# Kernel optimization log

Hardware: AMD Instinct MI355X
Metric: run time of the kernel (lower is better)

The kernel has to match this reference:

```python
import jax, jax.numpy as jnp
import numpy as np

LLR_CLIP = 20.0   # allowed_llr_range(abs=20)
QMAX = 7.5        # decoder_qms_qbit = 5 -> round(x*2)/2, clip +/-7.5


def _quantize_ste(x):
    # straight-through quantizer: forward = quantized, grad flows through clipped x
    q = jnp.clip(jnp.round(x * 2.0) / 2.0, -QMAX, QMAX)
    xc = jnp.clip(x, -QMAX, QMAX)
    return xc + jax.lax.stop_gradient(q - xc)


def _decode(xa, cn_weights, vn_idx, cn_idx, shifts, M):
    # xa: (B, Z, N) channel LLRs; messages live on lifted edges (B, Z, E)
    B, Z, N = xa.shape
    E = vn_idx.shape[0]
    iters = cn_weights.shape[0]

    zidx = jnp.arange(Z)
    lift = (zidx[:, None] + shifts[None, :]) % Z    # VN-domain -> CN-domain cyclic shift per edge
    unlift = (zidx[:, None] - shifts[None, :]) % Z  # inverse shift
    lift_b = jnp.broadcast_to(lift[None], (B, Z, E))
    unlift_b = jnp.broadcast_to(unlift[None], (B, Z, E))

    V = jax.nn.one_hot(vn_idx, N, dtype=xa.dtype)   # (E, N) edge->VN incidence (= W_output / W_skipconn2even)
    eids = jnp.arange(E)
    llr_e = xa[:, :, vn_idx]                        # per-edge channel LLR (B, Z, E)

    c2v = jnp.zeros((B, Z, E), xa.dtype)
    for it in range(iters):
        # --- VN update (odd layer): extrinsic sum + channel LLR, clipped ---
        tot = jnp.einsum('bze,en->bzn', c2v, V)                 # per-VN sum of incoming c2v
        v2c = jnp.clip(llr_e + tot[:, :, vn_idx] - c2v, -LLR_CLIP, LLR_CLIP)

        # --- lift to CN domain (Lift_Matrix1) ---
        m = jnp.take_along_axis(v2c, lift_b, axis=1)            # (B, Z, E)
        mt = m.transpose(2, 0, 1).reshape(E, B * Z)             # edges leading for segment ops

        # --- CN update (even layer): extrinsic min-sum via two-min trick ---
        a = jnp.abs(mt)
        neg = (mt < 0).astype(jnp.int32)
        min1 = jax.ops.segment_min(a, cn_idx, num_segments=M)               # (M, B*Z)
        ismin = a == min1[cn_idx]
        first = jax.ops.segment_min(jnp.where(ismin, eids[:, None], E),
                                    cn_idx, num_segments=M)                 # tie-break by edge id
        isfirst = eids[:, None] == first[cn_idx]
        min2 = jax.ops.segment_min(jnp.where(isfirst, jnp.inf, a),
                                   cn_idx, num_segments=M)
        ext_min = jnp.where(isfirst, min2[cn_idx], min1[cn_idx])
        negtot = jax.ops.segment_sum(neg, cn_idx, num_segments=M)
        sgn = (1 - 2 * ((negtot[cn_idx] - neg) % 2)).astype(mt.dtype)       # extrinsic sign product

        msg = _quantize_ste(cn_weights[it] * sgn * ext_min)     # per-iteration scalar CN weight + QMS quantize

        # --- unlift back to VN domain (Lift_Matrix2) ---
        mc = msg.reshape(E, B, Z).transpose(1, 2, 0)
        c2v = jnp.take_along_axis(mc, unlift_b, axis=1)

    # marginal output LLRs (W_output): channel + all incoming c2v, shape (B, N*Z)
    out = xa + jnp.einsum('bze,en->bzn', c2v, V)
    return out.transpose(0, 2, 1).reshape(B, N * Z)


def setup_inputs() -> dict:
    key = jax.random.key(0)
    B, Z, N, M, dc = 32, 384, 68, 46, 7
    E = M * dc  # 322
    k1, k2, k3 = jax.random.split(key, 3)
    xa = jax.random.normal(k1, (B, Z, N), dtype=jnp.float32) * 4.0
    cn_weights = jnp.ones((8,), jnp.float32)
    cn_idx = jnp.repeat(jnp.arange(M), dc)                      # regular CN degree 7
    vn_idx = jax.random.randint(k2, (E,), 0, N)
    shifts = jax.random.randint(k3, (E,), 0, Z)
    return {"xa": xa, "cn_weights": cn_weights, "vn_idx": vn_idx,
            "cn_idx": cn_idx, "shifts": shifts, "M": M}


def reference(xa, cn_weights, vn_idx, cn_idx, shifts, M):
    return _decode(xa, cn_weights, vn_idx, cn_idx, shifts, M)
```

## Files before the change

kernel.cpp:

```cpp
#include <hip/hip_runtime.h>

#define B_   32
#define Z_   384
#define N_   68
#define M_   46
#define DC_  7
#define E_   (M_ * DC_)
#define ZN   (Z_ * N_)
#define ZM   (Z_ * M_)

#define XAT_OFF   0
#define LT_OFF    (B_ * ZN)
#define MSG_OFF   (2 * B_ * ZN)
#define EVS_OFF   (MSG_OFF + 2 * B_ * ZM)
#define OFFS_OFF  (EVS_OFF + E_)
#define LST_OFF   (OFFS_OFF + N_ + 1)
#define WS_INTS   (LST_OFF + E_)


__global__ __launch_bounds__(384)
void k_pre_tables(const float* __restrict__ xa,
                  const int* __restrict__ vn_idx, const int* __restrict__ shifts,
                  int* __restrict__ ws, float* __restrict__ xat_dst)
{
    const int tid = threadIdx.x;
    if (blockIdx.x == B_ * 6) {
        __shared__ int evs[E_];
        __shared__ int offs[N_ + 1];
        __shared__ int lists[E_];
        if (tid < E_) evs[tid] = vn_idx[tid] | (shifts[tid] << 7);
        __syncthreads();
        if (tid < N_) {
            int c = 0;
            for (int e = 0; e < E_; ++e) c += ((evs[e] & 127) == tid);
            offs[tid + 1] = c;
        }
        if (tid == 0) offs[0] = 0;
        __syncthreads();
        if (tid == 0) { for (int n = 0; n < N_; ++n) offs[n + 1] += offs[n]; }
        __syncthreads();
        if (tid < N_) {
            int p = offs[tid];
            for (int e = 0; e < E_; ++e) {
                int rec = evs[e];
                if ((rec & 127) == tid) {
                    int s = rec >> 7;
                    lists[p++] = s | ((e / DC_) << 9) | ((e % DC_) << 15);
                }
            }
        }
        __syncthreads();
        if (tid < E_) { ws[EVS_OFF + tid] = evs[tid]; ws[LST_OFF + tid] = lists[tid]; }
        if (tid < N_ + 1) ws[OFFS_OFF + tid] = offs[tid];
        return;
    }
    __shared__ float tile[N_ * 65];
    const int x = blockIdx.x & 7;
    const int k = blockIdx.x >> 3;
    const int b = x + 8 * (k & 3);
    const int t = k >> 2;
    const int z0 = t * 64;
    const float* src = xa + (size_t)b * ZN + (size_t)z0 * N_;
    for (int i = tid; i < 64 * N_; i += 384) {
        int r = i / N_, n = i - r * N_;
        tile[n * 65 + r] = src[i];
    }
    __syncthreads();
    float* dst = xat_dst + (size_t)b * ZN + z0;
    for (int i = tid; i < 64 * N_; i += 384) {
        int n = i >> 6, zl = i & 63;
        dst[n * Z_ + zl] = tile[n * 65 + zl];
    }
}

__global__ __launch_bounds__(384)
void k_passB(const float* __restrict__ cw, const int* __restrict__ ws_tbl,
             int2* __restrict__ msg, const float* __restrict__ src_g,
             int it, int use_init)
{
    __shared__ int cevs[DC_];
    const int x = blockIdx.x & 7;
    const int k = blockIdx.x >> 3;
    const int b = x + 8 * (k & 3);
    const int m = k >> 2;
    const int z = threadIdx.x;
    if (z < DC_) cevs[z] = ws_tbl[EVS_OFF + m * DC_ + z];
    __syncthreads();

    const float* src = src_g + (size_t)b * ZN;
    int2* mp = msg + (size_t)b * ZM + m * Z_;
    const int2 old = use_init ? make_int2(0, 0) : mp[z];
    const float w = cw[it];

    float m1 = 1e30f, m2 = 1e30f;
    int f = 0, negb = 0;
    #pragma unroll
    for (int j = 0; j < DC_; ++j) {
        int rec = cevs[j];
        int vn = rec & 127;
        int s  = rec >> 7;
        int zr = z + s; if (zr >= Z_) zr -= Z_;
        int w32 = (j < 4) ? old.x : old.y;
        int c2 = (w32 << (24 - 8 * (j & 3))) >> 24;
        float v = src[vn * Z_ + zr] - 0.5f * (float)c2;
        v = fminf(fmaxf(v, -20.0f), 20.0f);
        negb |= (v < 0.0f) << j;
        float a = fabsf(v);
        if (a < m1) { m2 = m1; m1 = a; f = j; }
        else if (a < m2) { m2 = a; }
    }
    float r1 = fminf(fmaxf(rintf(w * m1 * 2.0f), -15.0f), 15.0f);
    float r2 = fminf(fmaxf(rintf(w * m2 * 2.0f), -15.0f), 15.0f);
    const int q1 = (int)r1, q2 = (int)r2;
    const int par = __popc(negb);
    int lo = 0, hi = 0;
    #pragma unroll
    for (int j = 0; j < DC_; ++j) {
        int q  = (j == f) ? q2 : q1;
        int sj = (par - ((negb >> j) & 1)) & 1;
        int mj = sj ? -q : q;
        if (j < 4) lo |= (mj & 255) << (8 * j);
        else       hi |= (mj & 255) << (8 * (j - 4));
    }
    mp[z] = make_int2(lo, hi);
}

__global__ __launch_bounds__(384)
void k_passA(const float* __restrict__ xat, const int* __restrict__ ws_tbl,
             const int2* __restrict__ msg, float* __restrict__ dst)
{
    __shared__ int vlist[E_];
    __shared__ int s_cnt;
    const int x = blockIdx.x & 7;
    const int k = blockIdx.x >> 3;
    const int b = x + 8 * (k & 3);
    const int n = k >> 2;
    const int tid = threadIdx.x;
    if (tid == 0) s_cnt = ws_tbl[OFFS_OFF + n + 1] - ws_tbl[OFFS_OFF + n];
    {
        int o = ws_tbl[OFFS_OFF + n];
        int e = ws_tbl[OFFS_OFF + n + 1];
        for (int q = o + tid; q < e; q += 384) vlist[q - o] = ws_tbl[LST_OFF + q];
    }
    __syncthreads();

    const int z = tid;
    const signed char* mb = (const signed char*)(msg + (size_t)b * ZM);
    const int cnt = s_cnt;
    int t2 = 0;
    for (int q = 0; q < cnt; ++q) {
        int rec = vlist[q];
        int s = rec & 511;
        int m = (rec >> 9) & 63;
        int j = (rec >> 15) & 7;
        int zs = z - s; if (zs < 0) zs += Z_;
        t2 += (int)mb[((m * Z_ + zs) << 3) + j];
    }
    dst[(size_t)b * ZN + n * Z_ + z] =
        xat[(size_t)b * ZN + n * Z_ + z] + 0.5f * (float)t2;
}

#define INIT_STATE ((16u << 10) | (16u << 15))
__device__ __forceinline__ int decode2(unsigned st, int j) {
    int neg   = (st >> j) & 1;
    int q1    = (int)((st >> 10) & 31) - 16;
    int q2    = (int)((st >> 15) & 31) - 16;
    int first = (int)((st >> 7) & 7);
    int q     = (j == first) ? q2 : q1;
    int par   = (__popc(st & 127u) - neg) & 1;
    return par ? -q : q;
}

__global__ __launch_bounds__(1024)
void ldpc_decode_kernel(const float* __restrict__ xa,
                        const float* __restrict__ cw,
                        const int*   __restrict__ vn_idx,
                        const int*   __restrict__ shifts,
                        float* out, int iters)
{
    __shared__ short tot[ZN];
    __shared__ int   evs[E_];
    __shared__ int   offs[N_ + 1];
    __shared__ int   lists[E_];
    __shared__ float wlds[8];

    const int tid = threadIdx.x;
    const int b   = blockIdx.x;
    const float* xab = xa + (size_t)b * ZN;
    float* outb = out + (size_t)b * ZN;
    int* stateg = (int*)outb;

    if (tid < E_) evs[tid] = vn_idx[tid] | (shifts[tid] << 7);
    if (tid < iters && tid < 8) wlds[tid] = cw[tid];
    __syncthreads();
    if (tid < N_) {
        int c = 0;
        for (int e = 0; e < E_; ++e) c += ((evs[e] & 127) == tid);
        offs[tid + 1] = c;
    }
    if (tid == 0) offs[0] = 0;
    __syncthreads();
    if (tid == 0) { for (int n = 0; n < N_; ++n) offs[n + 1] += offs[n]; }
    __syncthreads();
    if (tid < N_) {
        int p = offs[tid];
        for (int e = 0; e < E_; ++e) {
            int rec = evs[e];
            if ((rec & 127) == tid) {
                int s = rec >> 7;
                lists[p++] = s | ((e / DC_) << 9) | ((e % DC_) << 15);
            }
        }
    }
    __syncthreads();

    for (int i = tid; i < ZM; i += 1024) stateg[i] = (int)INIT_STATE;
    __syncthreads();

    for (int it = 0; it < iters; ++it) {
        for (int i = tid; i < ZN; i += 1024) {
            int z = i / N_, n = i - z * N_, t2 = 0;
            int kend = offs[n + 1];
            for (int k = offs[n]; k < kend; ++k) {
                int rec = lists[k];
                int s = rec & 511, m = (rec >> 9) & 63, j = rec >> 15;
                int zs = z - s; if (zs < 0) zs += Z_;
                t2 += decode2((unsigned)stateg[zs * M_ + m], j);
            }
            tot[i] = (short)t2;
        }
        __syncthreads();
        const float w = wlds[it];
        for (int i = tid; i < ZM; i += 1024) {
            int z = i / M_, m = i - z * M_;
            unsigned st = (unsigned)stateg[i];
            float m1 = 1e30f, m2 = 1e30f;
            int f = 0, negb = 0;
            #pragma unroll
            for (int j = 0; j < DC_; ++j) {
                int rec = evs[m * DC_ + j];
                int vn = rec & 127, s = rec >> 7;
                int zr = z + s; if (zr >= Z_) zr -= Z_;
                int c2 = decode2(st, j);
                int idx = zr * N_ + vn;
                float v = (xab[idx] + 0.5f * (float)tot[idx]) - 0.5f * (float)c2;
                v = fminf(fmaxf(v, -20.0f), 20.0f);
                negb |= (v < 0.0f) << j;
                float a = fabsf(v);
                if (a < m1) { m2 = m1; m1 = a; f = j; }
                else if (a < m2) { m2 = a; }
            }
            float r1 = fminf(fmaxf(rintf(w * m1 * 2.0f), -15.0f), 15.0f);
            float r2 = fminf(fmaxf(rintf(w * m2 * 2.0f), -15.0f), 15.0f);
            stateg[i] = (int)(unsigned)(negb | (f << 7) | (((int)r1 + 16) << 10) | (((int)r2 + 16) << 15));
        }
        __syncthreads();
    }

    for (int i = tid; i < ZN; i += 1024) {
        int z = i / N_, n = i - z * N_, t2 = 0;
        int kend = offs[n + 1];
        for (int k = offs[n]; k < kend; ++k) {
            int rec = lists[k];
            int s = rec & 511, m = (rec >> 9) & 63, j = rec >> 15;
            int zs = z - s; if (zs < 0) zs += Z_;
            t2 += decode2((unsigned)stateg[zs * M_ + m], j);
        }
        tot[i] = (short)t2;
    }
    __syncthreads();
    for (int i = tid; i < ZN; i += 1024) {
        int n = i / Z_, z = i - n * Z_;
        outb[i] = xab[z * N_ + n] + 0.5f * (float)tot[z * N_ + n];
    }
}

extern "C" void kernel_launch(void* const* d_in, const int* in_sizes, int n_in,
                              void* d_out, int out_size, void* d_ws, size_t ws_size,
                              hipStream_t stream) {
    const float* xa = (const float*)d_in[0];
    const float* cw = (const float*)d_in[1];
    const int* vn   = (const int*)d_in[2];
    const int* sh   = (const int*)d_in[4];
    int iters = in_sizes[1];
    float* outp = (float*)d_out;

    if (ws_size >= (size_t)WS_INTS * sizeof(int)) {
        int*   ws  = (int*)d_ws;
        float* xat = (float*)d_ws + XAT_OFF;
        float* lt  = (float*)d_ws + LT_OFF;
        int2*  msg = (int2*)(ws + MSG_OFF);

        if (iters == 0) {
            hipLaunchKernelGGL(k_pre_tables, dim3(B_ * 6 + 1), dim3(384), 0, stream,
                               xa, vn, sh, ws, outp);
            return;
        }
        hipLaunchKernelGGL(k_pre_tables, dim3(B_ * 6 + 1), dim3(384), 0, stream,
                           xa, vn, sh, ws, xat);
        hipLaunchKernelGGL(k_passB, dim3(B_ * M_), dim3(384), 0, stream,
                           cw, ws, msg, xat, 0, 1);
        for (int it = 1; it < iters; ++it) {
            hipLaunchKernelGGL(k_passA, dim3(B_ * N_), dim3(384), 0, stream,
                               xat, ws, msg, lt);
            hipLaunchKernelGGL(k_passB, dim3(B_ * M_), dim3(384), 0, stream,
                               cw, ws, msg, lt, it, 0);
        }
        hipLaunchKernelGGL(k_passA, dim3(B_ * N_), dim3(384), 0, stream,
                           xat, ws, msg, outp);
    } else {
        hipLaunchKernelGGL(ldpc_decode_kernel, dim3(B_), dim3(1024), 0, stream,
                           xa, cw, vn, sh, outp, iters);
    }
}
```

Baseline: 202.0 us.

## Replace per-iteration kernel launches with a persistent cooperative kernel using grid barriers

The per-iteration passA/passB launch sequence is replaced by one cooperative persistent kernel of 256 blocks × 1024 threads. Each block handles one slice of one batch and alternates VN and CN passes, separated by an atomic-counter grid barrier stored in the workspace. The aim is to remove the launch overhead and inter-kernel gaps of about 16 small launches. In exchange, each pass now runs on fewer blocks with a strided loop, and every phase pays barrier spin latency. Correctness depends on all 256 blocks being co-resident.

```diff
diff --git a/kernel.cpp b/kernel.cpp
--- a/kernel.cpp
+++ b/kernel.cpp
@@ -8,6 +8,9 @@
 #define E_   (M_ * DC_)
 #define ZN   (Z_ * N_)
 #define ZM   (Z_ * M_)
+#define GB_  256
+#define ZN_S (ZN / 8)
+#define ZM_S (ZM / 8)
 
 #define XAT_OFF   0
 #define LT_OFF    (B_ * ZN)
@@ -15,7 +18,8 @@
 #define EVS_OFF   (MSG_OFF + 2 * B_ * ZM)
 #define OFFS_OFF  (EVS_OFF + E_)
 #define LST_OFF   (OFFS_OFF + N_ + 1)
-#define WS_INTS   (LST_OFF + E_)
+#define BAR_OFF   (LST_OFF + E_)
+#define WS_INTS   (BAR_OFF + 2)
 
 
 __global__ __launch_bounds__(384)
@@ -29,6 +33,7 @@
         __shared__ int offs[N_ + 1];
         __shared__ int lists[E_];
         if (tid < E_) evs[tid] = vn_idx[tid] | (shifts[tid] << 7);
+        if (tid == 0) { ws[BAR_OFF] = 0; ws[BAR_OFF + 1] = 0; }
         __syncthreads();
         if (tid < N_) {
             int c = 0;
@@ -73,91 +78,135 @@
     }
 }
 
-__global__ __launch_bounds__(384)
-void k_passB(const float* __restrict__ cw, const int* __restrict__ ws_tbl,
-             int2* __restrict__ msg, const float* __restrict__ src_g,
-             int it, int use_init)
-{
-    __shared__ int cevs[DC_];
-    const int x = blockIdx.x & 7;
-    const int k = blockIdx.x >> 3;
-    const int b = x + 8 * (k & 3);
-    const int m = k >> 2;
-    const int z = threadIdx.x;
-    if (z < DC_) cevs[z] = ws_tbl[EVS_OFF + m * DC_ + z];
-    __syncthreads();
-
+__device__ __forceinline__ void gbar(unsigned* cnt, unsigned* gen, unsigned phase)
+{
+    __syncthreads();
+    if (threadIdx.x == 0) {
+        __threadfence();
+        unsigned old = __hip_atomic_fetch_add(cnt, 1u, __ATOMIC_ACQ_REL,
+                                              __HIP_MEMORY_SCOPE_AGENT);
+        if (old == (unsigned)gridDim.x - 1u) {
+            __hip_atomic_store(cnt, 0u, __ATOMIC_RELAXED, __HIP_MEMORY_SCOPE_AGENT);
+            __hip_atomic_store(gen, phase, __ATOMIC_RELEASE, __HIP_MEMORY_SCOPE_AGENT);
+        } else {
+            while (__hip_atomic_load(gen, __ATOMIC_ACQUIRE,
+                                     __HIP_MEMORY_SCOPE_AGENT) < phase) {
+                __builtin_amdgcn_s_sleep(2);
+            }
+        }
+        __threadfence();
+    }
+    __syncthreads();
+}
+
+__device__ __forceinline__ void passB_slice(int b, int sl,
+                                            const float* __restrict__ src_g,
+                                            int2* __restrict__ msg, float w,
+                                            const int* __restrict__ evs,
+                                            int use_init, int tid)
+{
     const float* src = src_g + (size_t)b * ZN;
-    int2* mp = msg + (size_t)b * ZM + m * Z_;
-    const int2 old = use_init ? make_int2(0, 0) : mp[z];
-    const float w = cw[it];
-
-    float m1 = 1e30f, m2 = 1e30f;
-    int f = 0, negb = 0;
-    #pragma unroll
-    for (int j = 0; j < DC_; ++j) {
-        int rec = cevs[j];
-        int vn = rec & 127;
-        int s  = rec >> 7;
-        int zr = z + s; if (zr >= Z_) zr -= Z_;
-        int w32 = (j < 4) ? old.x : old.y;
-        int c2 = (w32 << (24 - 8 * (j & 3))) >> 24;
-        float v = src[vn * Z_ + zr] - 0.5f * (float)c2;
-        v = fminf(fmaxf(v, -20.0f), 20.0f);
-        negb |= (v < 0.0f) << j;
-        float a = fabsf(v);
-        if (a < m1) { m2 = m1; m1 = a; f = j; }
-        else if (a < m2) { m2 = a; }
-    }
-    float r1 = fminf(fmaxf(rintf(w * m1 * 2.0f), -15.0f), 15.0f);
-    float r2 = fminf(fmaxf(rintf(w * m2 * 2.0f), -15.0f), 15.0f);
-    const int q1 = (int)r1, q2 = (int)r2;
-    const int par = __popc(negb);
-    int lo = 0, hi = 0;
-    #pragma unroll
-    for (int j = 0; j < DC_; ++j) {
-        int q  = (j == f) ? q2 : q1;
-        int sj = (par - ((negb >> j) & 1)) & 1;
-        int mj = sj ? -q : q;
-        if (j < 4) lo |= (mj & 255) << (8 * j);
-        else       hi |= (mj & 255) << (8 * (j - 4));
-    }
-    mp[z] = make_int2(lo, hi);
-}
-
-__global__ __launch_bounds__(384)
-void k_passA(const float* __restrict__ xat, const int* __restrict__ ws_tbl,
-             const int2* __restrict__ msg, float* __restrict__ dst)
-{
-    __shared__ int vlist[E_];
-    __shared__ int s_cnt;
-    const int x = blockIdx.x & 7;
-    const int k = blockIdx.x >> 3;
-    const int b = x + 8 * (k & 3);
-    const int n = k >> 2;
+    int2* mpb = msg + (size_t)b * ZM;
+    const int lo = sl * ZM_S, hi = lo + ZM_S;
+    for (int l = lo + tid; l < hi; l += 1024) {
+        const int m = l / Z_;
+        const int z = l - m * Z_;
+        const int2 old = use_init ? make_int2(0, 0) : mpb[l];
+
+        float m1 = 1e30f, m2 = 1e30f;
+        int f = 0, negb = 0;
+        #pragma unroll
+        for (int j = 0; j < DC_; ++j) {
+            int rec = evs[m * DC_ + j];
+            int vn = rec & 127;
+            int s  = rec >> 7;
+            int zr = z + s; if (zr >= Z_) zr -= Z_;
+            int w32 = (j < 4) ? old.x : old.y;
+            int c2 = (w32 << (24 - 8 * (j & 3))) >> 24;
+            float v = src[vn * Z_ + zr] - 0.5f * (float)c2;
+            v = fminf(fmaxf(v, -20.0f), 20.0f);
+            negb |= (v < 0.0f) << j;
+            float a = fabsf(v);
+            if (a < m1) { m2 = m1; m1 = a; f = j; }
+            else if (a < m2) { m2 = a; }
+        }
+        float r1 = fminf(fmaxf(rintf(w * m1 * 2.0f), -15.0f), 15.0f);
+        float r2 = fminf(fmaxf(rintf(w * m2 * 2.0f), -15.0f), 15.0f);
+        const int q1 = (int)r1, q2 = (int)r2;
+        const int par = __popc(negb);
+        int plo = 0, phi = 0;
+        #pragma unroll
+        for (int j = 0; j < DC_; ++j) {
+            int q  = (j == f) ? q2 : q1;
+            int sj = (par - ((negb >> j) & 1)) & 1;
+            int mj = sj ? -q : q;
+            if (j < 4) plo |= (mj & 255) << (8 * j);
+            else       phi |= (mj & 255) << (8 * (j - 4));
+        }
+        mpb[l] = make_int2(plo, phi);
+    }
+}
+
+__device__ __forceinline__ void passA_slice(int b, int sl,
+                                            const float* __restrict__ xat,
+                                            const int2* __restrict__ msg,
+                                            float* __restrict__ dst,
+                                            const int* __restrict__ offs,
+                                            const int* __restrict__ lists, int tid)
+{
+    const signed char* mb = (const signed char*)(msg + (size_t)b * ZM);
+    const float* xb = xat + (size_t)b * ZN;
+    float* db = dst + (size_t)b * ZN;
+    const int lo = sl * ZN_S, hi = lo + ZN_S;
+    for (int l = lo + tid; l < hi; l += 1024) {
+        const int n = l / Z_;
+        const int z = l - n * Z_;
+        const int o = offs[n], e = offs[n + 1];
+        int t2 = 0;
+        for (int k = o; k < e; ++k) {
+            int rec = lists[k];
+            int s = rec & 511;
+            int m = (rec >> 9) & 63;
+            int j = (rec >> 15) & 7;
+            int zs = z - s; if (zs < 0) zs += Z_;
+            t2 += (int)mb[((m * Z_ + zs) << 3) + j];
+        }
+        db[l] = xb[l] + 0.5f * (float)t2;
+    }
+}
+
+__global__ __launch_bounds__(1024)
+void k_persist(const float* __restrict__ xat, const float* __restrict__ cw,
+               int* __restrict__ ws, int2* __restrict__ msg,
+               float* __restrict__ lt, float* __restrict__ out, int iters)
+{
+    __shared__ int evs[E_];
+    __shared__ int lists[E_];
+    __shared__ int offs[N_ + 1];
+    __shared__ float wlds[8];
     const int tid = threadIdx.x;
-    if (tid == 0) s_cnt = ws_tbl[OFFS_OFF + n + 1] - ws_tbl[OFFS_OFF + n];
-    {
-        int o = ws_tbl[OFFS_OFF + n];
-        int e = ws_tbl[OFFS_OFF + n + 1];
-        for (int q = o + tid; q < e; q += 384) vlist[q - o] = ws_tbl[LST_OFF + q];
-    }
-    __syncthreads();
-
-    const int z = tid;
-    const signed char* mb = (const signed char*)(msg + (size_t)b * ZM);
-    const int cnt = s_cnt;
-    int t2 = 0;
-    for (int q = 0; q < cnt; ++q) {
-        int rec = vlist[q];
-        int s = rec & 511;
-        int m = (rec >> 9) & 63;
-        int j = (rec >> 15) & 7;
-        int zs = z - s; if (zs < 0) zs += Z_;
-        t2 += (int)mb[((m * Z_ + zs) << 3) + j];
-    }
-    dst[(size_t)b * ZN + n * Z_ + z] =
-        xat[(size_t)b * ZN + n * Z_ + z] + 0.5f * (float)t2;
+    if (tid < E_) { evs[tid] = ws[EVS_OFF + tid]; lists[tid] = ws[LST_OFF + tid]; }
+    if (tid < N_ + 1) offs[tid] = ws[OFFS_OFF + tid];
+    if (tid < 8 && tid < iters) wlds[tid] = cw[tid];
+    __syncthreads();
+
+    const int x  = blockIdx.x & 7;
+    const int kk = blockIdx.x >> 3;
+    const int b  = x + 8 * (kk & 3);
+    const int sl = kk >> 2;
+    unsigned* cnt = (unsigned*)(ws + BAR_OFF);
+    unsigned* gen = (unsigned*)(ws + BAR_OFF + 1);
+    unsigned phase = 0;
+
+    passB_slice(b, sl, xat, msg, wlds[0], evs, 1, tid);
+    for (int it = 1; it < iters; ++it) {
+        gbar(cnt, gen, ++phase);
+        passA_slice(b, sl, xat, msg, lt, offs, lists, tid);
+        gbar(cnt, gen, ++phase);
+        passB_slice(b, sl, lt, msg, wlds[it], evs, 0, tid);
+    }
+    gbar(cnt, gen, ++phase);
+    passA_slice(b, sl, xat, msg, out, offs, lists, tid);
 }
 
 #define INIT_STATE ((16u << 10) | (16u << 15))
@@ -298,16 +347,10 @@
         }
         hipLaunchKernelGGL(k_pre_tables, dim3(B_ * 6 + 1), dim3(384), 0, stream,
                            xa, vn, sh, ws, xat);
-        hipLaunchKernelGGL(k_passB, dim3(B_ * M_), dim3(384), 0, stream,
-                           cw, ws, msg, xat, 0, 1);
-        for (int it = 1; it < iters; ++it) {
-            hipLaunchKernelGGL(k_passA, dim3(B_ * N_), dim3(384), 0, stream,
-                               xat, ws, msg, lt);
-            hipLaunchKernelGGL(k_passB, dim3(B_ * M_), dim3(384), 0, stream,
-                               cw, ws, msg, lt, it, 0);
-        }
-        hipLaunchKernelGGL(k_passA, dim3(B_ * N_), dim3(384), 0, stream,
-                           xat, ws, msg, outp);
+        void* args[] = { (void*)&xat, (void*)&cw, (void*)&ws, (void*)&msg,
+                         (void*)&lt, (void*)&outp, (void*)&iters };
+        hipLaunchCooperativeKernel((const void*)k_persist, dim3(GB_), dim3(1024),
+                                   args, 0, stream);
     } else {
         hipLaunchKernelGGL(ldpc_decode_kernel, dim3(B_), dim3(1024), 0, stream,
                            xa, cw, vn, sh, outp, iters);
```

Result: slower. 665.6 us (+229.4%).

## Store CN messages as planar int8 arrays per edge slot, precompute offsets

Applied to the files above, without the earlier changes.

Replaces the packed int2 per-(b,m,z) message layout, eight bytes with one padding, by a planar byte layout indexed by edge slot j, then m, then z. The tables now carry precomputed base offsets (vn*Z, j*ZM+m*Z) so both passes skip the unpacking arithmetic. passA's byte gathers become contiguous across z, so reads coalesce instead of using a stride of eight bytes. The cost is that passB now issues seven separate byte loads and stores per thread instead of one 8-byte access.

```diff
diff --git a/kernel.cpp b/kernel.cpp
--- a/kernel.cpp
+++ b/kernel.cpp
@@ -8,11 +8,13 @@
 #define E_   (M_ * DC_)
 #define ZN   (Z_ * N_)
 #define ZM   (Z_ * M_)
+#define MSB  (DC_ * ZM)
 
 #define XAT_OFF   0
 #define LT_OFF    (B_ * ZN)
 #define MSG_OFF   (2 * B_ * ZN)
-#define EVS_OFF   (MSG_OFF + 2 * B_ * ZM)
+#define MSG_INTS  ((B_ * MSB + 3) / 4)
+#define EVS_OFF   (MSG_OFF + MSG_INTS)
 #define OFFS_OFF  (EVS_OFF + E_)
 #define LST_OFF   (OFFS_OFF + N_ + 1)
 #define WS_INTS   (LST_OFF + E_)
@@ -25,33 +27,33 @@
 {
     const int tid = threadIdx.x;
     if (blockIdx.x == B_ * 6) {
-        __shared__ int evs[E_];
+        __shared__ int vnl[E_];
+        __shared__ int shl[E_];
         __shared__ int offs[N_ + 1];
-        __shared__ int lists[E_];
-        if (tid < E_) evs[tid] = vn_idx[tid] | (shifts[tid] << 7);
+        if (tid < E_) { vnl[tid] = vn_idx[tid]; shl[tid] = shifts[tid]; }
         __syncthreads();
         if (tid < N_) {
             int c = 0;
-            for (int e = 0; e < E_; ++e) c += ((evs[e] & 127) == tid);
+            for (int e = 0; e < E_; ++e) c += (vnl[e] == tid);
             offs[tid + 1] = c;
         }
         if (tid == 0) offs[0] = 0;
         __syncthreads();
         if (tid == 0) { for (int n = 0; n < N_; ++n) offs[n + 1] += offs[n]; }
         __syncthreads();
+        if (tid < E_) {
+            ws[EVS_OFF + tid] = (vnl[tid] * Z_ << 9) | shl[tid];
+        }
+        if (tid < N_ + 1) ws[OFFS_OFF + tid] = offs[tid];
         if (tid < N_) {
             int p = offs[tid];
             for (int e = 0; e < E_; ++e) {
-                int rec = evs[e];
-                if ((rec & 127) == tid) {
-                    int s = rec >> 7;
-                    lists[p++] = s | ((e / DC_) << 9) | ((e % DC_) << 15);
+                if (vnl[e] == tid) {
+                    int m = e / DC_, j = e - m * DC_;
+                    ws[LST_OFF + p++] = ((j * ZM + m * Z_) << 9) | shl[e];
                 }
             }
         }
-        __syncthreads();
-        if (tid < E_) { ws[EVS_OFF + tid] = evs[tid]; ws[LST_OFF + tid] = lists[tid]; }
-        if (tid < N_ + 1) ws[OFFS_OFF + tid] = offs[tid];
         return;
     }
     __shared__ float tile[N_ * 65];
@@ -75,7 +77,7 @@
 
 __global__ __launch_bounds__(384)
 void k_passB(const float* __restrict__ cw, const int* __restrict__ ws_tbl,
-             int2* __restrict__ msg, const float* __restrict__ src_g,
+             signed char* __restrict__ msg, const float* __restrict__ src_g,
              int it, int use_init)
 {
     __shared__ int cevs[DC_];
@@ -88,8 +90,7 @@
     __syncthreads();
 
     const float* src = src_g + (size_t)b * ZN;
-    int2* mp = msg + (size_t)b * ZM + m * Z_;
-    const int2 old = use_init ? make_int2(0, 0) : mp[z];
+    signed char* mp = msg + (size_t)b * MSB + m * Z_ + z;
     const float w = cw[it];
 
     float m1 = 1e30f, m2 = 1e30f;
@@ -97,12 +98,10 @@
     #pragma unroll
     for (int j = 0; j < DC_; ++j) {
         int rec = cevs[j];
-        int vn = rec & 127;
-        int s  = rec >> 7;
+        int s = rec & 511;
         int zr = z + s; if (zr >= Z_) zr -= Z_;
-        int w32 = (j < 4) ? old.x : old.y;
-        int c2 = (w32 << (24 - 8 * (j & 3))) >> 24;
-        float v = src[vn * Z_ + zr] - 0.5f * (float)c2;
+        int c2 = use_init ? 0 : (int)mp[j * ZM];
+        float v = src[(rec >> 9) + zr] - 0.5f * (float)c2;
         v = fminf(fmaxf(v, -20.0f), 20.0f);
         negb |= (v < 0.0f) << j;
         float a = fabsf(v);
@@ -113,48 +112,40 @@
     float r2 = fminf(fmaxf(rintf(w * m2 * 2.0f), -15.0f), 15.0f);
     const int q1 = (int)r1, q2 = (int)r2;
     const int par = __popc(negb);
-    int lo = 0, hi = 0;
     #pragma unroll
     for (int j = 0; j < DC_; ++j) {
         int q  = (j == f) ? q2 : q1;
         int sj = (par - ((negb >> j) & 1)) & 1;
-        int mj = sj ? -q : q;
-        if (j < 4) lo |= (mj & 255) << (8 * j);
-        else       hi |= (mj & 255) << (8 * (j - 4));
-    }
-    mp[z] = make_int2(lo, hi);
+        mp[j * ZM] = (signed char)(sj ? -q : q);
+    }
 }
 
 __global__ __launch_bounds__(384)
 void k_passA(const float* __restrict__ xat, const int* __restrict__ ws_tbl,
-             const int2* __restrict__ msg, float* __restrict__ dst)
+             const signed char* __restrict__ msg, float* __restrict__ dst)
 {
-    __shared__ int vlist[E_];
+    __shared__ int vlist[16];
     __shared__ int s_cnt;
     const int x = blockIdx.x & 7;
     const int k = blockIdx.x >> 3;
     const int b = x + 8 * (k & 3);
     const int n = k >> 2;
     const int tid = threadIdx.x;
-    if (tid == 0) s_cnt = ws_tbl[OFFS_OFF + n + 1] - ws_tbl[OFFS_OFF + n];
-    {
-        int o = ws_tbl[OFFS_OFF + n];
-        int e = ws_tbl[OFFS_OFF + n + 1];
-        for (int q = o + tid; q < e; q += 384) vlist[q - o] = ws_tbl[LST_OFF + q];
-    }
+    const int o = ws_tbl[OFFS_OFF + n];
+    const int e = ws_tbl[OFFS_OFF + n + 1];
+    if (tid == 0) s_cnt = e - o;
+    if (tid < e - o && tid < 16) vlist[tid] = ws_tbl[LST_OFF + o + tid];
     __syncthreads();
 
     const int z = tid;
-    const signed char* mb = (const signed char*)(msg + (size_t)b * ZM);
+    const signed char* mb = msg + (size_t)b * MSB;
     const int cnt = s_cnt;
     int t2 = 0;
     for (int q = 0; q < cnt; ++q) {
-        int rec = vlist[q];
+        int rec = (q < 16) ? vlist[q] : ws_tbl[LST_OFF + o + q];
         int s = rec & 511;
-        int m = (rec >> 9) & 63;
-        int j = (rec >> 15) & 7;
         int zs = z - s; if (zs < 0) zs += Z_;
-        t2 += (int)mb[((m * Z_ + zs) << 3) + j];
+        t2 += (int)mb[(rec >> 9) + zs];
     }
     dst[(size_t)b * ZN + n * Z_ + z] =
         xat[(size_t)b * ZN + n * Z_ + z] + 0.5f * (float)t2;
@@ -286,10 +277,10 @@
     float* outp = (float*)d_out;
 
     if (ws_size >= (size_t)WS_INTS * sizeof(int)) {
-        int*   ws  = (int*)d_ws;
-        float* xat = (float*)d_ws + XAT_OFF;
-        float* lt  = (float*)d_ws + LT_OFF;
-        int2*  msg = (int2*)(ws + MSG_OFF);
+        int*         ws  = (int*)d_ws;
+        float*       xat = (float*)d_ws + XAT_OFF;
+        float*       lt  = (float*)d_ws + LT_OFF;
+        signed char* msg = (signed char*)(ws + MSG_OFF);
 
         if (iters == 0) {
             hipLaunchKernelGGL(k_pre_tables, dim3(B_ * 6 + 1), dim3(384), 0, stream,
```

Result: no change. 201.5 us (-0.3%).
